# Performance work log

Measured on AMD Instinct MI355X. Metric: run time of the kernel, lower is better.

## Reference

```python
import jax, jax.numpy as jnp
import numpy as np

K = 5       # strip kernel size
DIL = 1     # dilation
G = 4       # groups


def _strip_att(x, conv_w, inside_all, lamb_l, lamb_h, horizontal):
    # x: (n, c, h, w); conv_w: (G*K, c); inside_all: (c,1,1); lamb_*: (c,)
    n, c, h, w = x.shape
    # global avg pool -> 1x1 conv -> tanh filter, shaped (n, G, 1, K, 1, 1)
    f = jnp.tanh(jnp.einsum('nc,oc->no', x.mean(axis=(2, 3)), conv_w))
    f = f.reshape(n, G, 1, K, 1, 1)
    pad = DIL * (K - 1) // 2
    if horizontal:
        xp = jnp.pad(x, ((0, 0), (0, 0), (0, 0), (pad, pad)), mode='reflect')
        # K shifted strips along W (equivalent to F.unfold with kernel (1,K))
        wins = jnp.stack([xp[:, :, :, i * DIL:i * DIL + w] for i in range(K)], axis=2)
        gapx = x.mean(axis=3, keepdims=True)   # (n,c,h,1)
    else:
        xp = jnp.pad(x, ((0, 0), (0, 0), (pad, pad), (0, 0)), mode='reflect')
        wins = jnp.stack([xp[:, :, i * DIL:i * DIL + h, :] for i in range(K)], axis=2)
        gapx = x.mean(axis=2, keepdims=True)   # (n,c,1,w)
    # (n,c,K,h,w) -> (n,G,c//G,K,h,w); weighted sum over kernel positions
    wins = wins.reshape(n, G, c // G, K, h, w)
    out = (wins * f).sum(axis=3).reshape(n, c, h, w)
    out_low = (out * (inside_all + 1.0) - inside_all * gapx) * lamb_l[:, None, None]
    out_high = x * (lamb_h[:, None, None] + 1.0)
    return out_low + out_high


def setup_inputs() -> dict:
    key = jax.random.key(0)
    ks = jax.random.split(key, 11)
    C = 128
    x = jax.random.normal(ks[0], (4, C, 256, 256), dtype=jnp.float32)
    s = 0.1
    return {
        'x': x,
        'conv_h': jax.random.normal(ks[1], (G * K, C), dtype=jnp.float32) * s,
        'inside_h': jax.random.normal(ks[2], (C, 1, 1), dtype=jnp.float32) * s,
        'lamb_l_h': jax.random.normal(ks[3], (C,), dtype=jnp.float32) * s,
        'lamb_h_h': jax.random.normal(ks[4], (C,), dtype=jnp.float32) * s,
        'conv_v': jax.random.normal(ks[5], (G * K, C), dtype=jnp.float32) * s,
        'inside_v': jax.random.normal(ks[6], (C, 1, 1), dtype=jnp.float32) * s,
        'lamb_l_v': jax.random.normal(ks[7], (C,), dtype=jnp.float32) * s,
        'lamb_h_v': jax.random.normal(ks[8], (C,), dtype=jnp.float32) * s,
        'gamma': jax.random.normal(ks[9], (C, 1, 1), dtype=jnp.float32) * s,
        'beta': 1.0 + jax.random.normal(ks[10], (C, 1, 1), dtype=jnp.float32) * s,
    }


def reference(x, conv_h, inside_h, lamb_l_h, lamb_h_h,
              conv_v, inside_v, lamb_l_v, lamb_h_v, gamma, beta):
    out = _strip_att(x, conv_h, inside_h, lamb_l_h, lamb_h_h, horizontal=True)
    out = _strip_att(out, conv_v, inside_v, lamb_l_v, lamb_h_v, horizontal=False)
    return gamma * out + x * beta
```

## Files before the change

### kernel.cpp

```cpp
#include <hip/hip_runtime.h>
#include <math.h>

#define NB   4
#define CC   128
#define HH   256
#define WW   256
#define HWSZ (HH * WW)
#define NC   (NB * CC)
#define GK   20

__device__ __forceinline__ float wave_reduce_sum(float v) {
#pragma unroll
    for (int o = 1; o < 64; o <<= 1) v += __shfl_xor(v, o, 64);
    return v;
}

__global__ __launch_bounds__(256) void k_reduce(const float4* __restrict__ x4,
                                                float* __restrict__ rowsum,
                                                float* __restrict__ colsum,
                                                float* __restrict__ planesum) {
    const int b = blockIdx.x;
    const int t = threadIdx.x;
    const int wv = t >> 6;
    const int l = t & 63;
    const float4* plane = x4 + (size_t)b * (HWSZ / 4);
    const int r0 = wv * 64;

    float4 cs = make_float4(0.f, 0.f, 0.f, 0.f);
    for (int it = 0; it < 16; ++it) {
        const int r = r0 + 4 * it;
        float4 v0 = plane[(r + 0) * (WW / 4) + l];
        float4 v1 = plane[(r + 1) * (WW / 4) + l];
        float4 v2 = plane[(r + 2) * (WW / 4) + l];
        float4 v3 = plane[(r + 3) * (WW / 4) + l];
        cs.x += (v0.x + v1.x) + (v2.x + v3.x);
        cs.y += (v0.y + v1.y) + (v2.y + v3.y);
        cs.z += (v0.z + v1.z) + (v2.z + v3.z);
        cs.w += (v0.w + v1.w) + (v2.w + v3.w);
        float p0 = (v0.x + v0.y) + (v0.z + v0.w);
        float p1 = (v1.x + v1.y) + (v1.z + v1.w);
        float p2 = (v2.x + v2.y) + (v2.z + v2.w);
        float p3 = (v3.x + v3.y) + (v3.z + v3.w);
        p0 = wave_reduce_sum(p0);
        p1 = wave_reduce_sum(p1);
        p2 = wave_reduce_sum(p2);
        p3 = wave_reduce_sum(p3);
        if (l == 0) *(float4*)&rowsum[b * HH + r] = make_float4(p0, p1, p2, p3);
    }

    __shared__ float colpart[4][WW];
    colpart[wv][4 * l + 0] = cs.x;
    colpart[wv][4 * l + 1] = cs.y;
    colpart[wv][4 * l + 2] = cs.z;
    colpart[wv][4 * l + 3] = cs.w;
    __syncthreads();
    float c = (colpart[0][t] + colpart[1][t]) + (colpart[2][t] + colpart[3][t]);
    colsum[b * WW + t] = c;

    float p = wave_reduce_sum(c);
    __shared__ float pr[4];
    if (l == 0) pr[wv] = p;
    __syncthreads();
    if (t == 0) planesum[b] = (pr[0] + pr[1]) + (pr[2] + pr[3]);
}

__global__ __launch_bounds__(256) void k_small(const float* __restrict__ colsum,
                                               const float* __restrict__ planesum,
                                               const float* __restrict__ conv_h,
                                               const float* __restrict__ inside_h,
                                               const float* __restrict__ lamb_l_h,
                                               const float* __restrict__ lamb_h_h,
                                               const float* __restrict__ conv_v,
                                               float* __restrict__ f_h_out,
                                               float* __restrict__ f_v_out) {
    __shared__ float meanx[NC];
    __shared__ float fh[NB * GK];
    __shared__ float mo1[NC];
    const int t = threadIdx.x;

    for (int i = t; i < NC; i += 256) meanx[i] = planesum[i] * (1.f / HWSZ);
    __syncthreads();

    if (t < NB * GK) {
        const int n = t / GK, o = t % GK;
        float acc = 0.f;
        for (int c = 0; c < CC; ++c) acc += meanx[n * CC + c] * conv_h[o * CC + c];
        float v = tanhf(acc);
        fh[t] = v;
        f_h_out[t] = v;
    }
    __syncthreads();

    for (int i = t; i < NC; i += 256) {
        const int n = i >> 7, c = i & (CC - 1), g = c >> 5;
        const float* f = &fh[n * GK + g * 5];
        const float S = planesum[i];
        const float* col = colsum + i * WW;
        const float c0 = col[0], c1 = col[1], c2 = col[2];
        const float c253 = col[253], c254 = col[254], c255 = col[255];
        const float s0 = S + c1 + c2 - c254 - c255;
        const float s1 = S + c1 - c255;
        const float s2 = S;
        const float s3 = S + c254 - c0;
        const float s4 = S + c253 + c254 - c0 - c1;
        const float convmean =
            (f[0] * s0 + f[1] * s1 + f[2] * s2 + f[3] * s3 + f[4] * s4) * (1.f / HWSZ);
        const float A = (inside_h[c] + 1.f) * lamb_l_h[c];
        const float B = inside_h[c] * lamb_l_h[c];
        const float Cq = lamb_h_h[c] + 1.f;
        mo1[i] = A * convmean + (Cq - B) * meanx[i];
    }
    __syncthreads();

    if (t < NB * GK) {
        const int n = t / GK, o = t % GK;
        float acc = 0.f;
        for (int c = 0; c < CC; ++c) acc += mo1[n * CC + c] * conv_v[o * CC + c];
        f_v_out[t] = tanhf(acc);
    }
}

__global__ __launch_bounds__(256) void k_main(const float* __restrict__ x,
                                              const float* __restrict__ rowsum,
                                              const float* __restrict__ colsum,
                                              const float* __restrict__ planesum,
                                              const float* __restrict__ f_h,
                                              const float* __restrict__ f_v,
                                              const float* __restrict__ inside_h,
                                              const float* __restrict__ lamb_l_h,
                                              const float* __restrict__ lamb_h_h,
                                              const float* __restrict__ inside_v,
                                              const float* __restrict__ lamb_l_v,
                                              const float* __restrict__ lamb_h_v,
                                              const float* __restrict__ gamma,
                                              const float* __restrict__ beta,
                                              float* __restrict__ out) {
    const int b = blockIdx.x >> 1;
    const int half = blockIdx.x & 1;
    const int n = b >> 7, c = b & (CC - 1), g = c >> 5;
    const int t = threadIdx.x;
    const int wv = t >> 6;
    const int l = t & 63;

    float fh[5], fv[5];
#pragma unroll
    for (int k = 0; k < 5; ++k) {
        fh[k] = f_h[n * GK + g * 5 + k];
        fv[k] = f_v[n * GK + g * 5 + k];
    }
    const float Ah = (inside_h[c] + 1.f) * lamb_l_h[c];
    const float Bh = inside_h[c] * lamb_l_h[c];
    const float Ch = lamb_h_h[c] + 1.f;
    const float Av = (inside_v[c] + 1.f) * lamb_l_v[c];
    const float Bv = inside_v[c] * lamb_l_v[c];
    const float Cv = lamb_h_v[c] + 1.f;
    const float gm = gamma[c], bt = beta[c];
    const float meanx = planesum[b] * (1.f / HWSZ);

    __shared__ float lcol[WW + 4];
    lcol[t + 2] = colsum[b * WW + t] * (1.f / HH);
    if (t < 2) lcol[t] = colsum[b * WW + (2 - t)] * (1.f / HH);
    if (t >= WW - 2) lcol[t + 4] = colsum[b * WW + (2 * WW - 4 - t)] * (1.f / HH);
    __syncthreads();

    float Dg0, Dg1, Dg2, Dg3;
    {
        float q[8];
#pragma unroll
        for (int d = 0; d < 8; ++d) q[d] = lcol[4 * l + d];
        float gxv[4];
#pragma unroll
        for (int d = 0; d < 4; ++d) {
            gxv[d] = Ah * (fh[0] * q[d] + fh[1] * q[d + 1] + fh[2] * q[d + 2] +
                           fh[3] * q[d + 3] + fh[4] * q[d + 4]) -
                     Bh * meanx + Ch * q[d + 2];
        }
        const float nGB = -gm * Bv;
        Dg0 = nGB * gxv[0]; Dg1 = nGB * gxv[1];
        Dg2 = nGB * gxv[2]; Dg3 = nGB * gxv[3];
    }

    const float K4 = gm * Av * fv[4];
    const float K3 = gm * Av * fv[3];
    const float K2p = gm * (Av * fv[2] + Cv);
    const float K1 = gm * Av * fv[1];
    const float K0 = gm * Av * fv[0];

    const float* plane = x + (size_t)b * HWSZ;
    float* oplane = out + (size_t)b * HWSZ;
    const float* rsb = rowsum + b * HH;
    const int r0 = half * 128 + wv * 32;

    const int offa = (l == 0) ? 0 : 4 * l - 2;
    const int offb = (l == 63) ? 248 : 4 * l + 4;

    auto refl = [](int h) { return h < 0 ? -h : (h > HH - 1 ? 2 * HH - 2 - h : h); };

    int hr = refl(r0 - 2);
    const float* rp = plane + hr * WW;
    float4 v = *(const float4*)(rp + 4 * l);
    float2 a = *(const float2*)(rp + offa);
    float2 bb = *(const float2*)(rp + offb);
    float rs = rsb[hr];

    float4 acc0 = {0, 0, 0, 0}, acc1 = {0, 0, 0, 0};
    float4 acc2 = {0, 0, 0, 0}, acc3 = {0, 0, 0, 0};

    for (int i = 0; i < 36; ++i) {
        const float4 vc = v;
        const float2 ac = a, bc = bb;
        const float rsc = rs;
        if (i < 35) {
            const int h2 = refl(r0 - 1 + i);
            const float* rp2 = plane + h2 * WW;
            v = *(const float4*)(rp2 + 4 * l);
            a = *(const float2*)(rp2 + offa);
            bb = *(const float2*)(rp2 + offb);
            rs = rsb[h2];
        }
        const float gh = rsc * (1.f / WW);

        const float m2 = (l == 0) ? vc.z : ac.x;
        const float m1 = (l == 0) ? vc.y : ac.y;
        const float p4 = (l == 63) ? vc.z : bc.x;
        const float p5 = (l == 63) ? vc.y : bc.y;

        const float h0v = fh[0] * m2 + fh[1] * m1 + fh[2] * vc.x + fh[3] * vc.y + fh[4] * vc.z;
        const float h1v = fh[0] * m1 + fh[1] * vc.x + fh[2] * vc.y + fh[3] * vc.z + fh[4] * vc.w;
        const float h2v = fh[0] * vc.x + fh[1] * vc.y + fh[2] * vc.z + fh[3] * vc.w + fh[4] * p4;
        const float h3v = fh[0] * vc.y + fh[1] * vc.z + fh[2] * vc.w + fh[3] * p4 + fh[4] * p5;

        float4 hc;
        hc.x = Ah * h0v - Bh * gh + Ch * vc.x;
        hc.y = Ah * h1v - Bh * gh + Ch * vc.y;
        hc.z = Ah * h2v - Bh * gh + Ch * vc.z;
        hc.w = Ah * h3v - Bh * gh + Ch * vc.w;

        if (i >= 4) {
            float4 o;
            o.x = acc0.x + K4 * hc.x;
            o.y = acc0.y + K4 * hc.y;
            o.z = acc0.z + K4 * hc.z;
            o.w = acc0.w + K4 * hc.w;
            *(float4*)&oplane[(r0 + i - 4) * WW + 4 * l] = o;
        }
        acc0.x = acc1.x + K3 * hc.x;
        acc0.y = acc1.y + K3 * hc.y;
        acc0.z = acc1.z + K3 * hc.z;
        acc0.w = acc1.w + K3 * hc.w;
        acc1.x = acc2.x + K2p * hc.x + bt * vc.x;
        acc1.y = acc2.y + K2p * hc.y + bt * vc.y;
        acc1.z = acc2.z + K2p * hc.z + bt * vc.z;
        acc1.w = acc2.w + K2p * hc.w + bt * vc.w;
        acc2.x = acc3.x + K1 * hc.x;
        acc2.y = acc3.y + K1 * hc.y;
        acc2.z = acc3.z + K1 * hc.z;
        acc2.w = acc3.w + K1 * hc.w;
        acc3.x = K0 * hc.x + Dg0;
        acc3.y = K0 * hc.y + Dg1;
        acc3.z = K0 * hc.z + Dg2;
        acc3.w = K0 * hc.w + Dg3;
    }
}

extern "C" void kernel_launch(void* const* d_in, const int* in_sizes, int n_in,
                              void* d_out, int out_size, void* d_ws, size_t ws_size,
                              hipStream_t stream) {
    const float* x        = (const float*)d_in[0];
    const float* conv_h   = (const float*)d_in[1];
    const float* inside_h = (const float*)d_in[2];
    const float* lamb_l_h = (const float*)d_in[3];
    const float* lamb_h_h = (const float*)d_in[4];
    const float* conv_v   = (const float*)d_in[5];
    const float* inside_v = (const float*)d_in[6];
    const float* lamb_l_v = (const float*)d_in[7];
    const float* lamb_h_v = (const float*)d_in[8];
    const float* gamma    = (const float*)d_in[9];
    const float* beta     = (const float*)d_in[10];
    float* out = (float*)d_out;

    float* ws = (float*)d_ws;
    float* rowsum   = ws;
    float* colsum   = ws + 131072;
    float* planesum = ws + 262144;
    float* f_h      = ws + 262656;
    float* f_v      = ws + 262736;

    k_reduce<<<NC, 256, 0, stream>>>((const float4*)x, rowsum, colsum, planesum);
    k_small<<<1, 256, 0, stream>>>(colsum, planesum, conv_h, inside_h, lamb_l_h,
                                   lamb_h_h, conv_v, f_h, f_v);
    k_main<<<NC * 2, 256, 0, stream>>>(x, rowsum, colsum, planesum, f_h, f_v,
                                       inside_h, lamb_l_h, lamb_h_h,
                                       inside_v, lamb_l_v, lamb_h_v,
                                       gamma, beta, out);
}
```

Before: 84.46 us.

## Split main kernel into more row tiles, use lane shuffles for halos and nontemporal stores

```diff
diff --git a/kernel.cpp b/kernel.cpp
--- a/kernel.cpp
+++ b/kernel.cpp
@@ -8,6 +8,8 @@
 #define HWSZ (HH * WW)
 #define NC   (NB * CC)
 #define GK   20
+
+typedef float floatx4 __attribute__((ext_vector_type(4)));
 
 __device__ __forceinline__ float wave_reduce_sum(float v) {
 #pragma unroll
@@ -135,8 +137,8 @@
                                               const float* __restrict__ gamma,
                                               const float* __restrict__ beta,
                                               float* __restrict__ out) {
-    const int b = blockIdx.x >> 1;
-    const int half = blockIdx.x & 1;
+    const int b = blockIdx.x >> 2;
+    const int tile = blockIdx.x & 3;
     const int n = b >> 7, c = b & (CC - 1), g = c >> 5;
     const int t = threadIdx.x;
     const int wv = t >> 6;
@@ -189,41 +191,33 @@
     const float* plane = x + (size_t)b * HWSZ;
     float* oplane = out + (size_t)b * HWSZ;
     const float* rsb = rowsum + b * HH;
-    const int r0 = half * 128 + wv * 32;
-
-    const int offa = (l == 0) ? 0 : 4 * l - 2;
-    const int offb = (l == 63) ? 248 : 4 * l + 4;
+    const int r0 = tile * 64 + wv * 16;
 
     auto refl = [](int h) { return h < 0 ? -h : (h > HH - 1 ? 2 * HH - 2 - h : h); };
 
     int hr = refl(r0 - 2);
-    const float* rp = plane + hr * WW;
-    float4 v = *(const float4*)(rp + 4 * l);
-    float2 a = *(const float2*)(rp + offa);
-    float2 bb = *(const float2*)(rp + offb);
-    float rs = rsb[hr];
+    float4 v = *(const float4*)(plane + hr * WW + 4 * l);
+    float rs = rsb[__builtin_amdgcn_readfirstlane(hr)];
 
     float4 acc0 = {0, 0, 0, 0}, acc1 = {0, 0, 0, 0};
     float4 acc2 = {0, 0, 0, 0}, acc3 = {0, 0, 0, 0};
 
-    for (int i = 0; i < 36; ++i) {
+    for (int i = 0; i < 20; ++i) {
         const float4 vc = v;
-        const float2 ac = a, bc = bb;
         const float rsc = rs;
-        if (i < 35) {
+        if (i < 19) {
             const int h2 = refl(r0 - 1 + i);
-            const float* rp2 = plane + h2 * WW;
-            v = *(const float4*)(rp2 + 4 * l);
-            a = *(const float2*)(rp2 + offa);
-            bb = *(const float2*)(rp2 + offb);
-            rs = rsb[h2];
+            v = *(const float4*)(plane + h2 * WW + 4 * l);
+            rs = rsb[__builtin_amdgcn_readfirstlane(h2)];
         }
         const float gh = rsc * (1.f / WW);
 
-        const float m2 = (l == 0) ? vc.z : ac.x;
-        const float m1 = (l == 0) ? vc.y : ac.y;
-        const float p4 = (l == 63) ? vc.z : bc.x;
-        const float p5 = (l == 63) ? vc.y : bc.y;
+        float m2 = __shfl_up(vc.z, 1);
+        float m1 = __shfl_up(vc.w, 1);
+        float p4 = __shfl_down(vc.x, 1);
+        float p5 = __shfl_down(vc.y, 1);
+        if (l == 0)  { m2 = vc.z; m1 = vc.y; }
+        if (l == 63) { p4 = vc.z; p5 = vc.y; }
 
         const float h0v = fh[0] * m2 + fh[1] * m1 + fh[2] * vc.x + fh[3] * vc.y + fh[4] * vc.z;
         const float h1v = fh[0] * m1 + fh[1] * vc.x + fh[2] * vc.y + fh[3] * vc.z + fh[4] * vc.w;
@@ -237,12 +231,12 @@
         hc.w = Ah * h3v - Bh * gh + Ch * vc.w;
 
         if (i >= 4) {
-            float4 o;
+            floatx4 o;
             o.x = acc0.x + K4 * hc.x;
             o.y = acc0.y + K4 * hc.y;
             o.z = acc0.z + K4 * hc.z;
             o.w = acc0.w + K4 * hc.w;
-            *(float4*)&oplane[(r0 + i - 4) * WW + 4 * l] = o;
+            __builtin_nontemporal_store(o, (floatx4*)&oplane[(r0 + i - 4) * WW + 4 * l]);
         }
         acc0.x = acc1.x + K3 * hc.x;
         acc0.y = acc1.y + K3 * hc.y;
@@ -289,7 +283,7 @@
     k_reduce<<<NC, 256, 0, stream>>>((const float4*)x, rowsum, colsum, planesum);
     k_small<<<1, 256, 0, stream>>>(colsum, planesum, conv_h, inside_h, lamb_l_h,
                                    lamb_h_h, conv_v, f_h, f_v);
-    k_main<<<NC * 2, 256, 0, stream>>>(x, rowsum, colsum, planesum, f_h, f_v,
+    k_main<<<NC * 4, 256, 0, stream>>>(x, rowsum, colsum, planesum, f_h, f_v,
                                        inside_h, lamb_l_h, lamb_h_h,
                                        inside_v, lamb_l_v, lamb_h_v,
                                        gamma, beta, out);
```

Result: faster. 82.72 us (-2.1%).
